# Optimization experiments

Hardware: AMD Instinct MI355X
Metric: run time of the kernel (lower is better)

Reference implementation:

```python
import jax, jax.numpy as jnp
import numpy as np

N_BINS = 15


def setup_inputs() -> dict:
    key = jax.random.key(0)
    k1, k2 = jax.random.split(key)
    N = 33554432  # 32Mi elements
    logits = jax.random.normal(k1, (N,), dtype=jnp.float32) * 2.0
    labels = jax.random.randint(k2, (N,), 0, 2, dtype=jnp.int32)
    return {"logits": logits, "labels": labels}


def reference(logits, labels):
    # probs = sigmoid(logits); acc = (probs > 0.5) == labels
    probs = jax.nn.sigmoid(logits)
    acc = ((probs > 0.5).astype(labels.dtype) == labels).astype(probs.dtype)

    # Bins are (lower, upper] with edges = linspace(0, 1, n_bins+1).
    # digitize(..., right=True) gives i s.t. edges[i-1] < p <= edges[i].
    edges = jnp.linspace(0.0, 1.0, N_BINS + 1)
    idx = jnp.clip(jnp.digitize(probs, edges, right=True) - 1, 0, N_BINS - 1)
    # p == 0 falls in no bin in the original loop (first bin is (0, 1/15]).
    valid = (probs > edges[0]).astype(probs.dtype)

    # ece = sum_b |mean_conf_b - mean_acc_b| * (count_b / N)
    #     = sum_b |sum_conf_b - sum_acc_b| / N   (empty bins contribute 0)
    sum_conf = jax.ops.segment_sum(probs * valid, idx, num_segments=N_BINS)
    sum_acc = jax.ops.segment_sum(acc * valid, idx, num_segments=N_BINS)
    n = jnp.asarray(probs.size, probs.dtype)
    ece = jnp.sum(jnp.abs(sum_conf - sum_acc)) / n
    return ece.reshape(1)
```

## Files before the change

### kernel.cpp

```cpp
#include <hip/hip_runtime.h>

#define NBINS 15
#define NTHREADS 256
#define NWAVES 4
#define NBLOCKS 1024

__global__ __launch_bounds__(NTHREADS) void ece_partial_kernel(
    const float* __restrict__ logits,
    const int* __restrict__ labels,
    float* __restrict__ partials,
    int n)
{
    __shared__ float conf_lds[NWAVES][NBINS][64];
    __shared__ float accs_lds[NWAVES][NBINS][64];
    __shared__ float wavesum[2][NWAVES][NBINS];

    const int tid  = threadIdx.x;
    const int lane = tid & 63;
    const int w    = tid >> 6;

    #pragma unroll
    for (int b = 0; b < NBINS; ++b) {
        conf_lds[w][b][lane] = 0.0f;
        accs_lds[w][b][lane] = 0.0f;
    }

    const int n4 = n >> 2;
    const float4* L4 = (const float4*)logits;
    const int4*   Y4 = (const int4*)labels;
    const int stride = NBLOCKS * NTHREADS;

    for (int i = blockIdx.x * NTHREADS + tid; i < n4; i += stride) {
        float4 x = L4[i];
        int4   y = Y4[i];
        #pragma unroll
        for (int j = 0; j < 4; ++j) {
            float xv = (&x.x)[j];
            int   yv = (&y.x)[j];
            float p = 1.0f / (1.0f + __expf(-xv));
            int b = (int)ceilf(p * 15.0f) - 1;
            b = min(max(b, 0), NBINS - 1);
            if (p > 0.0f) {
                bool pred = p > 0.5f;
                float a = (pred == (yv != 0)) ? 1.0f : 0.0f;
                conf_lds[w][b][lane] += p;
                accs_lds[w][b][lane] += a;
            }
        }
    }

    if (blockIdx.x == 0) {
        for (int i = (n4 << 2) + tid; i < n; i += NTHREADS) {
            float xv = logits[i];
            int   yv = labels[i];
            float p = 1.0f / (1.0f + __expf(-xv));
            int b = (int)ceilf(p * 15.0f) - 1;
            b = min(max(b, 0), NBINS - 1);
            if (p > 0.0f) {
                bool pred = p > 0.5f;
                float a = (pred == (yv != 0)) ? 1.0f : 0.0f;
                conf_lds[w][b][lane] += p;
                accs_lds[w][b][lane] += a;
            }
        }
    }

    __syncthreads();

    #pragma unroll
    for (int b = 0; b < NBINS; ++b) {
        float c = conf_lds[w][b][lane];
        float a = accs_lds[w][b][lane];
        #pragma unroll
        for (int m = 32; m >= 1; m >>= 1) {
            c += __shfl_xor(c, m, 64);
            a += __shfl_xor(a, m, 64);
        }
        if (lane == 0) { wavesum[0][w][b] = c; wavesum[1][w][b] = a; }
    }
    __syncthreads();

    if (tid < 2 * NBINS) {
        const int arr = tid / NBINS;
        const int b   = tid % NBINS;
        float s = 0.0f;
        #pragma unroll
        for (int ww = 0; ww < NWAVES; ++ww) s += wavesum[arr][ww][b];
        partials[blockIdx.x * (2 * NBINS) + tid] = s;
    }
}

__global__ __launch_bounds__(NTHREADS) void ece_final_kernel(
    const float* __restrict__ partials,
    float* __restrict__ out,
    float inv_n)
{
    __shared__ double red[2 * NBINS];
    const int t = threadIdx.x;
    if (t < 8 * 2 * NBINS) {
        const int j   = t >> 3;
        const int sub = t & 7;
        double s = 0.0;
        for (int k = sub; k < NBLOCKS; k += 8)
            s += (double)partials[k * (2 * NBINS) + j];
        s += __shfl_xor(s, 4, 8);
        s += __shfl_xor(s, 2, 8);
        s += __shfl_xor(s, 1, 8);
        if (sub == 0) red[j] = s;
    }
    __syncthreads();
    if (t == 0) {
        double e = 0.0;
        #pragma unroll
        for (int b = 0; b < NBINS; ++b)
            e += fabs(red[b] - red[NBINS + b]);
        out[0] = (float)(e * (double)inv_n);
    }
}

extern "C" void kernel_launch(void* const* d_in, const int* in_sizes, int n_in,
                              void* d_out, int out_size, void* d_ws, size_t ws_size,
                              hipStream_t stream)
{
    const float* logits = (const float*)d_in[0];
    const int*   labels = (const int*)d_in[1];
    float* out      = (float*)d_out;
    float* partials = (float*)d_ws;
    const int n = in_sizes[0];

    ece_partial_kernel<<<NBLOCKS, NTHREADS, 0, stream>>>(logits, labels, partials, n);
    ece_final_kernel<<<1, NTHREADS, 0, stream>>>(partials, out, 1.0f / (float)n);
}
```

Baseline: 91.62 us.

## Replace LDS bin scatter with register cumulative-threshold sums

Instead of scattering confidence and accuracy into per-lane LDS histograms, each thread accumulates p-acc into 15 register cumulative sums gated by p > edge, and bins are recovered as differences of adjacent cumulative sums in the final kernel. This removes LDS read-modify-write traffic and halves the partials to reduce. Block count is doubled. It trades LDS latency for 15 compare/add ops per element and risks some fp32 cancellation error from differencing cumulative sums.

```diff
diff --git a/kernel.cpp b/kernel.cpp
--- a/kernel.cpp
+++ b/kernel.cpp
@@ -3,7 +3,7 @@
 #define NBINS 15
 #define NTHREADS 256
 #define NWAVES 4
-#define NBLOCKS 1024
+#define NBLOCKS 2048
 
 __global__ __launch_bounds__(NTHREADS) void ece_partial_kernel(
     const float* __restrict__ logits,
@@ -11,19 +11,13 @@
     float* __restrict__ partials,
     int n)
 {
-    __shared__ float conf_lds[NWAVES][NBINS][64];
-    __shared__ float accs_lds[NWAVES][NBINS][64];
-    __shared__ float wavesum[2][NWAVES][NBINS];
+    float S[NBINS];
+    #pragma unroll
+    for (int k = 0; k < NBINS; ++k) S[k] = 0.0f;
 
     const int tid  = threadIdx.x;
     const int lane = tid & 63;
     const int w    = tid >> 6;
-
-    #pragma unroll
-    for (int b = 0; b < NBINS; ++b) {
-        conf_lds[w][b][lane] = 0.0f;
-        accs_lds[w][b][lane] = 0.0f;
-    }
 
     const int n4 = n >> 2;
     const float4* L4 = (const float4*)logits;
@@ -38,13 +32,12 @@
             float xv = (&x.x)[j];
             int   yv = (&y.x)[j];
             float p = 1.0f / (1.0f + __expf(-xv));
-            int b = (int)ceilf(p * 15.0f) - 1;
-            b = min(max(b, 0), NBINS - 1);
-            if (p > 0.0f) {
-                bool pred = p > 0.5f;
-                float a = (pred == (yv != 0)) ? 1.0f : 0.0f;
-                conf_lds[w][b][lane] += p;
-                accs_lds[w][b][lane] += a;
+            float a = ((p > 0.5f) == (yv != 0)) ? 1.0f : 0.0f;
+            float t = p - a;
+            #pragma unroll
+            for (int k = 0; k < NBINS; ++k) {
+                const float edge = (float)k / 15.0f;
+                S[k] += (p > edge) ? t : 0.0f;
             }
         }
     }
@@ -54,39 +47,32 @@
             float xv = logits[i];
             int   yv = labels[i];
             float p = 1.0f / (1.0f + __expf(-xv));
-            int b = (int)ceilf(p * 15.0f) - 1;
-            b = min(max(b, 0), NBINS - 1);
-            if (p > 0.0f) {
-                bool pred = p > 0.5f;
-                float a = (pred == (yv != 0)) ? 1.0f : 0.0f;
-                conf_lds[w][b][lane] += p;
-                accs_lds[w][b][lane] += a;
+            float a = ((p > 0.5f) == (yv != 0)) ? 1.0f : 0.0f;
+            float t = p - a;
+            #pragma unroll
+            for (int k = 0; k < NBINS; ++k) {
+                const float edge = (float)k / 15.0f;
+                S[k] += (p > edge) ? t : 0.0f;
             }
         }
     }
 
-    __syncthreads();
-
+    __shared__ float wavesum[NWAVES][NBINS];
     #pragma unroll
-    for (int b = 0; b < NBINS; ++b) {
-        float c = conf_lds[w][b][lane];
-        float a = accs_lds[w][b][lane];
+    for (int k = 0; k < NBINS; ++k) {
+        float s = S[k];
         #pragma unroll
-        for (int m = 32; m >= 1; m >>= 1) {
-            c += __shfl_xor(c, m, 64);
-            a += __shfl_xor(a, m, 64);
-        }
-        if (lane == 0) { wavesum[0][w][b] = c; wavesum[1][w][b] = a; }
+        for (int m = 32; m >= 1; m >>= 1)
+            s += __shfl_xor(s, m, 64);
+        if (lane == 0) wavesum[w][k] = s;
     }
     __syncthreads();
 
-    if (tid < 2 * NBINS) {
-        const int arr = tid / NBINS;
-        const int b   = tid % NBINS;
+    if (tid < NBINS) {
         float s = 0.0f;
         #pragma unroll
-        for (int ww = 0; ww < NWAVES; ++ww) s += wavesum[arr][ww][b];
-        partials[blockIdx.x * (2 * NBINS) + tid] = s;
+        for (int ww = 0; ww < NWAVES; ++ww) s += wavesum[ww][tid];
+        partials[blockIdx.x * NBINS + tid] = s;
     }
 }
 
@@ -95,25 +81,27 @@
     float* __restrict__ out,
     float inv_n)
 {
-    __shared__ double red[2 * NBINS];
+    __shared__ double red[NBINS];
     const int t = threadIdx.x;
-    if (t < 8 * 2 * NBINS) {
-        const int j   = t >> 3;
-        const int sub = t & 7;
+    if (t < 16 * NBINS) {
+        const int b   = t >> 4;
+        const int sub = t & 15;
         double s = 0.0;
-        for (int k = sub; k < NBLOCKS; k += 8)
-            s += (double)partials[k * (2 * NBINS) + j];
-        s += __shfl_xor(s, 4, 8);
-        s += __shfl_xor(s, 2, 8);
-        s += __shfl_xor(s, 1, 8);
-        if (sub == 0) red[j] = s;
+        for (int k = sub; k < NBLOCKS; k += 16)
+            s += (double)partials[k * NBINS + b];
+        s += __shfl_xor(s, 8, 16);
+        s += __shfl_xor(s, 4, 16);
+        s += __shfl_xor(s, 2, 16);
+        s += __shfl_xor(s, 1, 16);
+        if (sub == 0) red[b] = s;
     }
     __syncthreads();
     if (t == 0) {
         double e = 0.0;
         #pragma unroll
-        for (int b = 0; b < NBINS; ++b)
-            e += fabs(red[b] - red[NBINS + b]);
+        for (int b = 0; b < NBINS - 1; ++b)
+            e += fabs(red[b] - red[b + 1]);
+        e += fabs(red[NBINS - 1]);
         out[0] = (float)(e * (double)inv_n);
     }
 }
```

Measured after the change: 97.43 us. 6.3% more time.
